# Performance work log

Measured on AMD Instinct MI355X. Metric: run time of the kernel, lower is better.

Reference implementation:

```python
import jax, jax.numpy as jnp
import numpy as np

N, E, E_LG, H, KGE, NUM_GRAPHS, N_ITER = 100000, 500000, 1000000, 128, 128, 1024, 2
EPS = 1e-5

def _prelu(x, a):
    return jnp.where(x >= 0, x, a * x)

def _seg_mean(vals, idx, num):
    s = jax.ops.segment_sum(vals, idx, num_segments=num)
    c = jax.ops.segment_sum(jnp.ones((vals.shape[0],), vals.dtype), idx, num_segments=num)
    return s / jnp.maximum(c, 1.0)[:, None]

def setup_inputs() -> dict:
    key = jax.random.key(0)
    ks = jax.random.split(key, 16)
    sc = 1.0 / np.sqrt(H)
    inp = {
        "x": jax.random.normal(ks[0], (N, H), jnp.float32),
        "edge_attr": jax.random.normal(ks[1], (E, H), jnp.float32),
        "edge_index": jax.random.randint(ks[2], (2, E), 0, N),
        "batch": jnp.sort(jax.random.randint(ks[3], (N,), 0, NUM_GRAPHS)),
        "line_graph_edge_index": jax.random.randint(ks[4], (2, E_LG), 0, E),
        # edge_update_net: Linear + PReLU + BatchNorm1d (eval mode)
        "W1": jax.random.normal(ks[5], (H, H), jnp.float32) * sc,
        "b1": jnp.zeros((H,), jnp.float32),
        "a1": jnp.full((1,), 0.25, jnp.float32),
        "bn_gamma": jnp.ones((H,), jnp.float32),
        "bn_beta": jnp.zeros((H,), jnp.float32),
        "bn_mean": jnp.zeros((H,), jnp.float32),
        "bn_var": jnp.ones((H,), jnp.float32),
        # GRU (single layer, single step)
        "w_ih": jax.random.normal(ks[6], (3 * H, H), jnp.float32) * sc,
        "w_hh": jax.random.normal(ks[7], (3 * H, H), jnp.float32) * sc,
        "b_ih": jnp.zeros((3 * H,), jnp.float32),
        "b_hh": jnp.zeros((3 * H,), jnp.float32),
        # DynamicAttention net
        "Wa1": jax.random.normal(ks[8], (H // 2, H), jnp.float32) * sc,
        "ba1": jnp.zeros((H // 2,), jnp.float32),
        "a2": jnp.full((1,), 0.25, jnp.float32),
        "Wa2": jax.random.normal(ks[9], (1, H // 2), jnp.float32) * (1.0 / np.sqrt(H // 2)),
        "ba2": jnp.zeros((1,), jnp.float32),
        # readout
        "Wr": jax.random.normal(ks[10], (KGE, H), jnp.float32) * sc,
        "br": jnp.zeros((KGE,), jnp.float32),
    }
    return inp

def reference(x, edge_attr, W1, b1, a1, bn_gamma, bn_beta, bn_mean, bn_var,
              w_ih, w_hh, b_ih, b_hh, Wa1, ba1, a2, Wa2, ba2, Wr, br,
              edge_index, batch, line_graph_edge_index):
    src, dst = edge_index[0], edge_index[1]
    l_src, l_dst = line_graph_edge_index[0], line_graph_edge_index[1]
    h = x  # GRU hidden state [N, H]
    for _ in range(N_ITER):
        # edge-to-edge message passing (node_to_edge_proj is Identity here)
        fused = edge_attr + (x[src] + x[dst]) * 0.5  # [E, H]
        agg = _seg_mean(fused[l_src], l_dst, E)      # scatter-mean over line graph
        upd = _prelu(agg @ W1.T + b1, a1)
        upd = (upd - bn_mean) * jax.lax.rsqrt(bn_var + EPS) * bn_gamma + bn_beta
        fused = fused + upd
        node_updates = _seg_mean(fused, dst, N)      # [N, H]
        # single GRU step
        gi = node_updates @ w_ih.T + b_ih
        gh = h @ w_hh.T + b_hh
        gi_r, gi_z, gi_n = jnp.split(gi, 3, axis=-1)
        gh_r, gh_z, gh_n = jnp.split(gh, 3, axis=-1)
        r = jax.nn.sigmoid(gi_r + gh_r)
        z = jax.nn.sigmoid(gi_z + gh_z)
        n = jnp.tanh(gi_n + r * gh_n)
        h = (1.0 - z) * n + z * h
        x = h
    # dynamic attention: per-graph scalar gate
    graph_repr = _seg_mean(x, batch, NUM_GRAPHS)     # [G, H]
    attn = jax.nn.sigmoid(_prelu(graph_repr @ Wa1.T + ba1, a2) @ Wa2.T + ba2)  # [G, 1]
    attended = x * attn[batch]
    graph_emb = jax.ops.segment_sum(attended, batch, num_segments=NUM_GRAPHS)
    graph_emb = graph_emb @ Wr.T + br
    return (x, graph_emb)
```

## Files before the change

### kernel.cpp

```cpp
#include <hip/hip_runtime.h>
#include <stdint.h>

#define H 128
#define G_NUM 1024
#define BN_EPS 1e-5f

typedef unsigned int uint;
typedef unsigned short ushort;
typedef __attribute__((ext_vector_type(8))) __bf16 bf16x8;
typedef __attribute__((ext_vector_type(8))) ushort ushort8;
typedef __attribute__((ext_vector_type(4))) float f32x4;

__device__ __forceinline__ float b2f(ushort u){ return __uint_as_float(((uint)u) << 16); }
__device__ __forceinline__ ushort f2b(float f){
    uint u = __float_as_uint(f);
    u += 0x7FFFu + ((u >> 16) & 1u);
    return (ushort)(u >> 16);
}
__device__ __forceinline__ float ldf(const void* p, size_t i, int bf){
    return bf ? b2f(((const ushort*)p)[i]) : ((const float*)p)[i];
}
__device__ __forceinline__ int swz(int r, int byte_in_row){
    return (r * 256 + byte_in_row) ^ ((r & 7) << 4);
}

__global__ void k_probe(const uint* __restrict__ gamma_bits, int* __restrict__ flag){
    if (threadIdx.x == 0 && blockIdx.x == 0)
        *flag = (gamma_bits[0] == 0x3F803F80u) ? 1 : 0;
}

__global__ __launch_bounds__(256) void k_count2(const int* __restrict__ lgi, const int* __restrict__ ei,
                                                int* __restrict__ cnt, int ELG, int E){
    int t = blockIdx.x * 256 + threadIdx.x;
    if (t < ELG) atomicAdd(&cnt[lgi[ELG + t]], 1);
    else { int t2 = t - ELG; if (t2 < E) atomicAdd(&cnt[E + ei[E + t2]], 1); }
}
__global__ __launch_bounds__(256) void k_scan_reduce(const int* __restrict__ cnt, int* __restrict__ bsum, int n){
    int base = blockIdx.x * 1024;
    int s = 0;
    for (int i = threadIdx.x; i < 1024; i += 256){ int idx = base + i; s += (idx < n) ? cnt[idx] : 0; }
    __shared__ int r[256];
    r[threadIdx.x] = s; __syncthreads();
    for (int o = 128; o > 0; o >>= 1){ if (threadIdx.x < o) r[threadIdx.x] += r[threadIdx.x + o]; __syncthreads(); }
    if (threadIdx.x == 0) bsum[blockIdx.x] = r[0];
}
__global__ __launch_bounds__(256) void k_scan_mid(int* __restrict__ bsum, int nb){
    __shared__ int ts[256];
    int tid = threadIdx.x;
    int loc[4]; int s = 0;
    #pragma unroll
    for (int j = 0; j < 4; j++){
        int idx = tid * 4 + j;
        loc[j] = s;
        s += (idx < nb) ? bsum[idx] : 0;
    }
    ts[tid] = s; __syncthreads();
    for (int o = 1; o < 256; o <<= 1){
        int v = (tid >= o) ? ts[tid - o] : 0;
        __syncthreads();
        ts[tid] += v;
        __syncthreads();
    }
    int texcl = ts[tid] - s;
    #pragma unroll
    for (int j = 0; j < 4; j++){
        int idx = tid * 4 + j;
        if (idx < nb) bsum[idx] = texcl + loc[j];
    }
}
__global__ __launch_bounds__(256) void k_scan_final(const int* __restrict__ cnt, const int* __restrict__ bsum,
                                                    int* __restrict__ off, int n){
    __shared__ int ts[256];
    int base = blockIdx.x * 1024;
    int tid = threadIdx.x;
    int loc[4]; int s = 0;
    #pragma unroll
    for (int j = 0; j < 4; j++){
        int idx = base + tid * 4 + j;
        loc[j] = s;
        s += (idx < n) ? cnt[idx] : 0;
    }
    ts[tid] = s; __syncthreads();
    for (int o = 1; o < 256; o <<= 1){
        int v = (tid >= o) ? ts[tid - o] : 0;
        __syncthreads();
        ts[tid] += v;
        __syncthreads();
    }
    int texcl = ts[tid] - s + bsum[blockIdx.x];
    #pragma unroll
    for (int j = 0; j < 4; j++){
        int idx = base + tid * 4 + j;
        if (idx < n) off[idx] = texcl + loc[j];
    }
}
__global__ void k_sent1(int* __restrict__ off, int idx, int val){
    if (threadIdx.x == 0) off[idx] = val;
}
__global__ __launch_bounds__(256) void k_fill2(const int* __restrict__ lgi, const int* __restrict__ ei,
                                               const int* __restrict__ off, int* __restrict__ cur,
                                               int* __restrict__ list, int ELG, int E){
    int t = blockIdx.x * 256 + threadIdx.x;
    if (t < ELG){
        int k = lgi[ELG + t];
        int pos = atomicAdd(&cur[k], 1);
        list[off[k] + pos] = lgi[t];
    } else {
        int t2 = t - ELG;
        if (t2 < E){
            int k = E + ei[E + t2];
            int pos = atomicAdd(&cur[k], 1);
            list[off[k] + pos] = t2;
        }
    }
}
__global__ void k_zero2(ushort* __restrict__ a, ushort* __restrict__ b, size_t off){
    int t = threadIdx.x;
    a[off + t] = 0; b[off + t] = 0;
}
__global__ __launch_bounds__(256) void k_cvt_bf(const void* __restrict__ in, ushort* __restrict__ out,
                                                int n, const int* __restrict__ flag){
    int t = blockIdx.x * 256 + threadIdx.x;
    if (t >= n) return;
    if (*flag) out[t] = ((const ushort*)in)[t];
    else       out[t] = f2b(((const float*)in)[t]);
}
__global__ __launch_bounds__(256) void k_wcvt(const void* __restrict__ W1, const void* __restrict__ wih,
                                              const void* __restrict__ whh,
                                              ushort* __restrict__ W1bf, ushort* __restrict__ wihbf,
                                              ushort* __restrict__ whhbf, const int* __restrict__ flag){
    int t = blockIdx.x * 256 + threadIdx.x;
    int bf = *flag;
    if (t < 16384) W1bf[t] = bf ? ((const ushort*)W1)[t] : f2b(((const float*)W1)[t]);
    else if (t < 65536){ int i = t - 16384; wihbf[i] = bf ? ((const ushort*)wih)[i] : f2b(((const float*)wih)[i]); }
    else if (t < 114688){ int i = t - 65536; whhbf[i] = bf ? ((const ushort*)whh)[i] : f2b(((const float*)whh)[i]); }
}
__global__ __launch_bounds__(256) void k_transpose(const void* __restrict__ in, float* __restrict__ out,
                                                   int R, int C, const int* __restrict__ flag){
    int t = blockIdx.x * 256 + threadIdx.x;
    if (t >= R * C) return;
    int bf = *flag;
    int r = t / C, c = t - r * C;
    out[c * R + r] = ldf(in, t, bf);
}
__global__ void k_params(const void* b1, const void* a1, const void* gam, const void* bet,
                         const void* mean, const void* var, const void* bih, const void* bhh,
                         float* __restrict__ ep, float* __restrict__ bi, float* __restrict__ bh,
                         const int* __restrict__ flag){
    int t = threadIdx.x; int bf = *flag;
    bi[t] = ldf(bih, t, bf);
    bh[t] = ldf(bhh, t, bf);
    if (t < 128){
        ep[t]       = ldf(b1, t, bf);
        ep[128 + t] = rsqrtf(ldf(var, t, bf) + BN_EPS) * ldf(gam, t, bf);
        ep[256 + t] = ldf(mean, t, bf);
        ep[384 + t] = ldf(bet, t, bf);
    }
    if (t == 0) ep[512] = ldf(a1, 0, bf);
}
__global__ __launch_bounds__(256) void k_store_h(const ushort* __restrict__ hb, void* __restrict__ out,
                                                 int n, const int* __restrict__ flag){
    int t = blockIdx.x * 256 + threadIdx.x;
    if (t >= n) return;
    ushort v = hb[t];
    if (*flag) ((ushort*)out)[t] = v;
    else       ((float*) out)[t] = b2f(v);
}

__global__ __launch_bounds__(256) void k_fused(const void* __restrict__ ea, const ushort* __restrict__ hb,
                                               const int* __restrict__ ei, ushort* __restrict__ fused,
                                               int E, const int* __restrict__ flag){
    int t = blockIdx.x * 256 + threadIdx.x;
    if (t >= E * 16) return;
    int bf = *flag;
    int e = t >> 4, ch = (t & 15) * 8;
    int s = ei[e], d = ei[E + e];
    ushort8 hs = *(const ushort8*)(hb + (size_t)s * H + ch);
    ushort8 hd = *(const ushort8*)(hb + (size_t)d * H + ch);
    size_t base = (size_t)e * H + ch;
    float av[8];
    if (bf){
        ushort8 a = *(const ushort8*)((const ushort*)ea + base);
        #pragma unroll
        for (int j = 0; j < 8; j++) av[j] = b2f(a[j]);
    } else {
        float4 a0 = *(const float4*)((const float*)ea + base);
        float4 a1 = *(const float4*)((const float*)ea + base + 4);
        av[0] = a0.x; av[1] = a0.y; av[2] = a0.z; av[3] = a0.w;
        av[4] = a1.x; av[5] = a1.y; av[6] = a1.z; av[7] = a1.w;
    }
    ushort8 o;
    #pragma unroll
    for (int j = 0; j < 8; j++) o[j] = f2b(av[j] + 0.5f * (b2f(hs[j]) + b2f(hd[j])));
    *(ushort8*)(fused + base) = o;
}

__global__ __launch_bounds__(256) void k_agg_gemm(const ushort* __restrict__ fused,
                                                  const int* __restrict__ off_cat, const int* __restrict__ list,
                                                  const ushort* __restrict__ W1bf, const float* __restrict__ ep,
                                                  ushort* __restrict__ fused2, int E, int LMAX){
    __shared__ __attribute__((aligned(16))) char As[32 * 256];
    __shared__ int offL[33];
    int tid = threadIdx.x, wid = tid >> 6, lane = tid & 63;
    int r0 = blockIdx.x * 32;
    if (tid < 33) offL[tid] = off_cat[r0 + tid];
    __syncthreads();
    int l16 = lane >> 4, ch16 = lane & 15;
    int rA = wid * 8 + l16, rB = rA + 4;
    int baseA = offL[rA], degA = offL[rA + 1] - baseA;
    int baseB = offL[rB], degB = offL[rB + 1] - baseB;
    int dm = max(degA, degB);
    float accA[8] = {}, accB[8] = {};
    #pragma unroll 4
    for (int i = 0; i < dm; i++){
        int liA = baseA + i; liA = (liA < LMAX) ? liA : (LMAX - 1);
        int liB = baseB + i; liB = (liB < LMAX) ? liB : (LMAX - 1);
        int sA = list[liA];
        int sB = list[liB];
        sA = (i < degA) ? sA : E;
        sB = (i < degB) ? sB : E;
        ushort8 vA = *(const ushort8*)(fused + (size_t)sA * H + ch16 * 8);
        ushort8 vB = *(const ushort8*)(fused + (size_t)sB * H + ch16 * 8);
        #pragma unroll
        for (int j = 0; j < 8; j++){ accA[j] += b2f(vA[j]); accB[j] += b2f(vB[j]); }
    }
    float invA = 1.f / fmaxf((float)degA, 1.f);
    float invB = 1.f / fmaxf((float)degB, 1.f);
    ushort8 oA, oB;
    #pragma unroll
    for (int j = 0; j < 8; j++){ oA[j] = f2b(accA[j] * invA); oB[j] = f2b(accB[j] * invB); }
    *(ushort8*)(As + swz(rA, ch16 * 16)) = oA;
    *(ushort8*)(As + swz(rB, ch16 * 16)) = oB;
    __syncthreads();
    int lrow = lane & 15, lhi = lane >> 4;
    f32x4 acc[2][2] = {};
    #pragma unroll
    for (int ks = 0; ks < 4; ks++){
        bf16x8 afr[2];
        #pragma unroll
        for (int rt = 0; rt < 2; rt++)
            afr[rt] = *(const bf16x8*)(As + swz(rt * 16 + lrow, ks * 64 + lhi * 16));
        #pragma unroll
        for (int cc = 0; cc < 2; cc++){
            int c = (2 * wid + cc) * 16 + lrow;
            bf16x8 bfr = *(const bf16x8*)(W1bf + (size_t)c * H + ks * 32 + lhi * 8);
            #pragma unroll
            for (int rt = 0; rt < 2; rt++)
                acc[cc][rt] = __builtin_amdgcn_mfma_f32_16x16x32_bf16(afr[rt], bfr, acc[cc][rt], 0, 0, 0);
        }
    }
    __syncthreads();
    float aa = ep[512];
    #pragma unroll
    for (int cc = 0; cc < 2; cc++){
        int c = (2 * wid + cc) * 16 + lrow;
        float bb = ep[c], sc = ep[128 + c], mb = ep[256 + c], be = ep[384 + c];
        #pragma unroll
        for (int rt = 0; rt < 2; rt++)
            #pragma unroll
            for (int rg = 0; rg < 4; rg++){
                int r = rt * 16 + lhi * 4 + rg;
                float u = acc[cc][rt][rg] + bb;
                u = (u >= 0.f) ? u : aa * u;
                u = (u - mb) * sc + be;
                *(ushort*)(As + swz(r, c * 2)) = f2b(u);
            }
    }
    __syncthreads();
    #pragma unroll
    for (int q = 0; q < 2; q++){
        int r = (q == 0) ? rA : rB;
        size_t gbase = (size_t)(r0 + r) * H + ch16 * 8;
        ushort8 f = *(const ushort8*)(fused + gbase);
        ushort8 u = *(const ushort8*)(As + swz(r, ch16 * 16));
        ushort8 o;
        #pragma unroll
        for (int j = 0; j < 8; j++) o[j] = f2b(b2f(f[j]) + b2f(u[j]));
        *(ushort8*)(fused2 + gbase) = o;
    }
}

__global__ __launch_bounds__(256) void k_gru(const ushort* __restrict__ fused2,
                                             const int* __restrict__ off_cat, const int* __restrict__ list,
                                             ushort* __restrict__ hb,
                                             const ushort* __restrict__ wihbf, const ushort* __restrict__ whhbf,
                                             const float* __restrict__ bi, const float* __restrict__ bh,
                                             int N, int EZ, int LMAX){
    __shared__ __attribute__((aligned(16))) char NUs[32 * 256];
    __shared__ __attribute__((aligned(16))) char HHs[32 * 256];
    __shared__ int offL[33];
    int tid = threadIdx.x, wid = tid >> 6, lane = tid & 63;
    int r0 = blockIdx.x * 32;
    if (tid < 33) offL[tid] = off_cat[r0 + tid];
    int l16 = lane >> 4, ch16 = lane & 15;
    int rA = wid * 8 + l16, rB = rA + 4;
    *(ushort8*)(HHs + swz(rA, ch16 * 16)) = *(const ushort8*)(hb + (size_t)(r0 + rA) * H + ch16 * 8);
    *(ushort8*)(HHs + swz(rB, ch16 * 16)) = *(const ushort8*)(hb + (size_t)(r0 + rB) * H + ch16 * 8);
    __syncthreads();
    int baseA = offL[rA], degA = offL[rA + 1] - baseA;
    int baseB = offL[rB], degB = offL[rB + 1] - baseB;
    int dm = max(degA, degB);
    float accA[8] = {}, accB[8] = {};
    #pragma unroll 4
    for (int i = 0; i < dm; i++){
        int liA = baseA + i; liA = (liA < LMAX) ? liA : (LMAX - 1);
        int liB = baseB + i; liB = (liB < LMAX) ? liB : (LMAX - 1);
        int sA = list[liA];
        int sB = list[liB];
        sA = (i < degA) ? sA : EZ;
        sB = (i < degB) ? sB : EZ;
        ushort8 vA = *(const ushort8*)(fused2 + (size_t)sA * H + ch16 * 8);
        ushort8 vB = *(const ushort8*)(fused2 + (size_t)sB * H + ch16 * 8);
        #pragma unroll
        for (int j = 0; j < 8; j++){ accA[j] += b2f(vA[j]); accB[j] += b2f(vB[j]); }
    }
    float invA = 1.f / fmaxf((float)degA, 1.f);
    float invB = 1.f / fmaxf((float)degB, 1.f);
    ushort8 oA, oB;
    #pragma unroll
    for (int j = 0; j < 8; j++){ oA[j] = f2b(accA[j] * invA); oB[j] = f2b(accB[j] * invB); }
    *(ushort8*)(NUs + swz(rA, ch16 * 16)) = oA;
    *(ushort8*)(NUs + swz(rB, ch16 * 16)) = oB;
    __syncthreads();
    int lrow = lane & 15, lhi = lane >> 4;
    ushort hnew[2][2][4];
    #pragma unroll
    for (int b = 0; b < 2; b++){
        f32x4 aI[3][2] = {}, aH[3][2] = {};
        #pragma unroll
        for (int ks = 0; ks < 4; ks++){
            bf16x8 fN[2], fH[2];
            #pragma unroll
            for (int rt = 0; rt < 2; rt++){
                int addr = swz(rt * 16 + lrow, ks * 64 + lhi * 16);
                fN[rt] = *(const bf16x8*)(NUs + addr);
                fH[rt] = *(const bf16x8*)(HHs + addr);
            }
            #pragma unroll
            for (int g = 0; g < 3; g++){
                int c = g * 128 + (wid + 4 * b) * 16 + lrow;
                bf16x8 bI = *(const bf16x8*)(wihbf + (size_t)c * H + ks * 32 + lhi * 8);
                bf16x8 bH = *(const bf16x8*)(whhbf + (size_t)c * H + ks * 32 + lhi * 8);
                #pragma unroll
                for (int rt = 0; rt < 2; rt++){
                    aI[g][rt] = __builtin_amdgcn_mfma_f32_16x16x32_bf16(fN[rt], bI, aI[g][rt], 0, 0, 0);
                    aH[g][rt] = __builtin_amdgcn_mfma_f32_16x16x32_bf16(fH[rt], bH, aH[g][rt], 0, 0, 0);
                }
            }
        }
        int c = (wid + 4 * b) * 16 + lrow;
        float bir = bi[c], biz = bi[128 + c], bin = bi[256 + c];
        float bhr = bh[c], bhz = bh[128 + c], bhn = bh[256 + c];
        #pragma unroll
        for (int rt = 0; rt < 2; rt++)
            #pragma unroll
            for (int rg = 0; rg < 4; rg++){
                int r = rt * 16 + lhi * 4 + rg;
                float gr = aI[0][rt][rg] + bir + aH[0][rt][rg] + bhr;
                float gz = aI[1][rt][rg] + biz + aH[1][rt][rg] + bhz;
                float rv = 1.f / (1.f + __expf(-gr));
                float zv = 1.f / (1.f + __expf(-gz));
                float nv = tanhf(aI[2][rt][rg] + bin + rv * (aH[2][rt][rg] + bhn));
                float hold = b2f(*(const ushort*)(HHs + swz(r, c * 2)));
                hnew[b][rt][rg] = f2b((1.f - zv) * nv + zv * hold);
            }
    }
    __syncthreads();
    #pragma unroll
    for (int b = 0; b < 2; b++){
        int c = (wid + 4 * b) * 16 + lrow;
        #pragma unroll
        for (int rt = 0; rt < 2; rt++)
            #pragma unroll
            for (int rg = 0; rg < 4; rg++){
                int r = rt * 16 + lhi * 4 + rg;
                *(ushort*)(NUs + swz(r, c * 2)) = hnew[b][rt][rg];
            }
    }
    __syncthreads();
    *(ushort8*)(hb + (size_t)(r0 + rA) * H + ch16 * 8) = *(const ushort8*)(NUs + swz(rA, ch16 * 16));
    *(ushort8*)(hb + (size_t)(r0 + rB) * H + ch16 * 8) = *(const ushort8*)(NUs + swz(rB, ch16 * 16));
}

__global__ __launch_bounds__(256) void k_gbounds(const int* __restrict__ batch, int* __restrict__ gs, int N, int G){
    int g = blockIdx.x * 256 + threadIdx.x;
    if (g > G) return;
    int lo = 0, hi = N;
    while (lo < hi){ int mid = (lo + hi) >> 1; if (batch[mid] < g) lo = mid + 1; else hi = mid; }
    gs[g] = lo;
}
__global__ __launch_bounds__(256) void k_graph_sum(const ushort* __restrict__ hb, const int* __restrict__ gs,
                                                   float* __restrict__ gsum){
    int g = blockIdx.x, c = threadIdx.x & 127, half = threadIdx.x >> 7;
    int s = gs[g], e = gs[g + 1];
    float acc0 = 0.f, acc1 = 0.f;
    int r = s + half;
    for (; r + 2 < e; r += 4){
        acc0 += b2f(hb[(size_t)r * H + c]);
        acc1 += b2f(hb[(size_t)(r + 2) * H + c]);
    }
    for (; r < e; r += 2) acc0 += b2f(hb[(size_t)r * H + c]);
    __shared__ float tmp[128];
    if (half == 1) tmp[c] = acc0 + acc1;
    __syncthreads();
    if (half == 0) gsum[(size_t)g * H + c] = acc0 + acc1 + tmp[c];
}
__global__ void k_attn(const float* __restrict__ gsum, const int* __restrict__ gs,
                       const void* __restrict__ Wa1, const void* __restrict__ ba1,
                       const void* __restrict__ a2, const void* __restrict__ Wa2,
                       const void* __restrict__ ba2, float* __restrict__ attn, const int* __restrict__ flag){
    int g = blockIdx.x;
    int j = threadIdx.x;
    int bf = *flag;
    float inv = 1.0f / fmaxf((float)(gs[g + 1] - gs[g]), 1.0f);
    __shared__ float R[H];
    for (int i = j; i < H; i += 64) R[i] = gsum[(size_t)g * H + i] * inv;
    __syncthreads();
    float t = 0.f;
    for (int k = 0; k < H; k++) t += R[k] * ldf(Wa1, (size_t)j * H + k, bf);
    t += ldf(ba1, j, bf);
    float al = ldf(a2, 0, bf);
    t = (t >= 0.f) ? t : al * t;
    float p = t * ldf(Wa2, j, bf);
    #pragma unroll
    for (int o = 32; o > 0; o >>= 1) p += __shfl_down(p, o);
    if (j == 0) attn[g] = 1.f / (1.f + __expf(-(p + ldf(ba2, 0, bf))));
}
__global__ __launch_bounds__(256) void k_graph_gemm(const float* __restrict__ gsum, const float* __restrict__ attn,
                                                    const float* __restrict__ WrT,
                                                    const void* __restrict__ br, void* __restrict__ out,
                                                    size_t obase, const int* __restrict__ flag){
    __shared__ float A[8 * H];
    int bf = *flag;
    int r0 = blockIdx.x * 8;
    for (int i = threadIdx.x; i < 8 * H; i += 256){
        int r = i >> 7;
        A[i] = gsum[(size_t)(r0 + r) * H + (i & 127)] * attn[r0 + r];
    }
    __syncthreads();
    int c = threadIdx.x & 127;
    int rr = (threadIdx.x >> 7) * 4;
    float acc[4] = {0, 0, 0, 0};
    for (int k = 0; k < H; k++){
        float w = WrT[k * H + c];
        #pragma unroll
        for (int j = 0; j < 4; j++) acc[j] += A[(rr + j) * H + k] * w;
    }
    float bb = ldf(br, c, bf);
    for (int j = 0; j < 4; j++){
        size_t idx = obase + (size_t)(r0 + rr + j) * H + c;
        float v = acc[j] + bb;
        if (bf) ((ushort*)out)[idx] = f2b(v);
        else    ((float*) out)[idx] = v;
    }
}

extern "C" void kernel_launch(void* const* d_in, const int* in_sizes, int n_in,
                              void* d_out, int out_size, void* d_ws, size_t ws_size,
                              hipStream_t stream)
{
    const void* x    = d_in[0];
    const void* ea   = d_in[1];
    const int*  ei   = (const int*)d_in[2];
    const int*  batch= (const int*)d_in[3];
    const int*  lgi  = (const int*)d_in[4];
    const void* W1   = d_in[5];
    const void* b1   = d_in[6];
    const void* a1   = d_in[7];
    const void* bng  = d_in[8];
    const void* bnb  = d_in[9];
    const void* bnm  = d_in[10];
    const void* bnv  = d_in[11];
    const void* wih  = d_in[12];
    const void* whh  = d_in[13];
    const void* bih  = d_in[14];
    const void* bhh  = d_in[15];
    const void* Wa1  = d_in[16];
    const void* ba1  = d_in[17];
    const void* a2   = d_in[18];
    const void* Wa2  = d_in[19];
    const void* ba2  = d_in[20];
    const void* Wr   = d_in[21];
    const void* br   = d_in[22];

    const int N   = in_sizes[0] / H;
    const int E   = in_sizes[1] / H;
    const int ELG = in_sizes[4] / 2;
    const int G   = G_NUM;
    const int NK  = E + N;
    const int nb  = (NK + 1023) / 1024;

    char* ws = (char*)d_ws;
    size_t off = 0;
    auto alloc = [&](size_t b) -> void* { void* p = ws + off; off += (b + 255) & ~(size_t)255; return p; };
    int*    flag    = (int*)   alloc(256);
    ushort* hb      = (ushort*)alloc((size_t)N * H * 2);
    ushort* fused   = (ushort*)alloc((size_t)(E + 1) * H * 2);
    ushort* fused2  = (ushort*)alloc((size_t)(E + 1) * H * 2);
    int*    zreg    = (int*)   alloc((size_t)(2 * NK) * 4);
    int*    cnt_cat = zreg;
    int*    cur_cat = zreg + NK;
    int*    off_cat = (int*)   alloc((size_t)(NK + 1) * 4);
    int*    list_cat= (int*)   alloc((size_t)(ELG + E) * 4);
    int*    bsum    = (int*)   alloc((size_t)(nb + 8) * 4);
    int*    gs      = (int*)   alloc((size_t)(G + 1) * 4);
    ushort* W1bf    = (ushort*)alloc(128 * 128 * 2);
    ushort* wihbf   = (ushort*)alloc(384 * 128 * 2);
    ushort* whhbf   = (ushort*)alloc(384 * 128 * 2);
    float*  ep      = (float*) alloc(513 * 4);
    float*  bi      = (float*) alloc(384 * 4);
    float*  bh      = (float*) alloc(384 * 4);
    float*  WrT     = (float*) alloc(128 * 128 * 4);
    float*  gsum    = (float*) alloc((size_t)G * H * 4);
    float*  attn    = (float*) alloc((size_t)G * 4);

    k_probe<<<1, 64, 0, stream>>>((const uint*)bng, flag);

    hipMemsetAsync(zreg, 0, (size_t)(2 * NK) * 4, stream);
    k_count2<<<(ELG + E + 255) / 256, 256, 0, stream>>>(lgi, ei, cnt_cat, ELG, E);
    k_scan_reduce<<<nb, 256, 0, stream>>>(cnt_cat, bsum, NK);
    k_scan_mid<<<1, 256, 0, stream>>>(bsum, nb);
    k_scan_final<<<nb, 256, 0, stream>>>(cnt_cat, bsum, off_cat, NK);
    k_sent1<<<1, 64, 0, stream>>>(off_cat, NK, ELG + E);
    k_fill2<<<(ELG + E + 255) / 256, 256, 0, stream>>>(lgi, ei, off_cat, cur_cat, list_cat, ELG, E);
    k_zero2<<<1, 128, 0, stream>>>(fused, fused2, (size_t)E * H);

    k_wcvt<<<(114688 + 255) / 256, 256, 0, stream>>>(W1, wih, whh, W1bf, wihbf, whhbf, flag);
    k_params<<<1, 384, 0, stream>>>(b1, a1, bng, bnb, bnm, bnv, bih, bhh, ep, bi, bh, flag);
    k_transpose<<<(128 * 128 + 255) / 256, 256, 0, stream>>>(Wr, WrT, 128, 128, flag);

    k_cvt_bf<<<(N * H + 255) / 256, 256, 0, stream>>>(x, hb, N * H, flag);

    for (int it = 0; it < 2; it++){
        k_fused<<<(E * 16 + 255) / 256, 256, 0, stream>>>(ea, hb, ei, fused, E, flag);
        k_agg_gemm<<<(E + 31) / 32, 256, 0, stream>>>(fused, off_cat, list_cat, W1bf, ep, fused2, E, ELG);
        k_gru<<<(N + 31) / 32, 256, 0, stream>>>(fused2, off_cat + E, list_cat, hb, wihbf, whhbf, bi, bh, N, E, ELG + E);
    }

    k_gbounds<<<(G + 256) / 256, 256, 0, stream>>>(batch, gs, N, G);
    k_graph_sum<<<G, 256, 0, stream>>>(hb, gs, gsum);
    k_attn<<<G, 64, 0, stream>>>(gsum, gs, Wa1, ba1, a2, Wa2, ba2, attn, flag);
    k_graph_gemm<<<G / 8, 256, 0, stream>>>(gsum, attn, WrT, br, d_out, (size_t)N * H, flag);
    k_store_h<<<(N * H + 255) / 256, 256, 0, stream>>>(hb, d_out, N * H, flag);
}
```

Before: 1.012 ms.

## Merge small setup kernels and vectorize bf16 gather accumulation with wave-uniform trip count

Folds the dtype probe, parameter prep, sentinel write and padding-row zeroing into one setup kernel, and moves the Wr transpose into the weight-conversion kernel. This cuts several tiny launches from the stream. The gather loops in the aggregation and GRU kernels now unpack bf16 pairs into packed float2 accumulators. Their loop bound is the maximum degree across the wave, so the trip count is uniform and the unroll factor drops from 4 to 2. The wave-wide maximum adds padded iterations for rows with fewer neighbours.

```diff
diff --git a/kernel.cpp b/kernel.cpp
--- a/kernel.cpp
+++ b/kernel.cpp
@@ -10,6 +10,7 @@
 typedef __attribute__((ext_vector_type(8))) __bf16 bf16x8;
 typedef __attribute__((ext_vector_type(8))) ushort ushort8;
 typedef __attribute__((ext_vector_type(4))) float f32x4;
+typedef __attribute__((ext_vector_type(2))) float f32x2;
 
 __device__ __forceinline__ float b2f(ushort u){ return __uint_as_float(((uint)u) << 16); }
 __device__ __forceinline__ ushort f2b(float f){
@@ -24,9 +25,31 @@
     return (r * 256 + byte_in_row) ^ ((r & 7) << 4);
 }
 
-__global__ void k_probe(const uint* __restrict__ gamma_bits, int* __restrict__ flag){
-    if (threadIdx.x == 0 && blockIdx.x == 0)
-        *flag = (gamma_bits[0] == 0x3F803F80u) ? 1 : 0;
+__global__ void k_setup_small(const uint* __restrict__ gamma_bits,
+                              const void* b1, const void* a1, const void* gam, const void* bet,
+                              const void* mean, const void* var, const void* bih, const void* bhh,
+                              float* __restrict__ ep, float* __restrict__ bi, float* __restrict__ bh,
+                              int* __restrict__ flag, ushort* __restrict__ fz1, ushort* __restrict__ fz2,
+                              size_t zoff, int* __restrict__ off_cat, int nk_idx, int sent_val){
+    __shared__ int bfs;
+    int t = threadIdx.x;
+    if (t == 0){
+        int f = (gamma_bits[0] == 0x3F803F80u) ? 1 : 0;
+        *flag = f; bfs = f;
+        off_cat[nk_idx] = sent_val;
+    }
+    __syncthreads();
+    int bf = bfs;
+    bi[t] = ldf(bih, t, bf);
+    bh[t] = ldf(bhh, t, bf);
+    if (t < 128){
+        ep[t]       = ldf(b1, t, bf);
+        ep[128 + t] = rsqrtf(ldf(var, t, bf) + BN_EPS) * ldf(gam, t, bf);
+        ep[256 + t] = ldf(mean, t, bf);
+        ep[384 + t] = ldf(bet, t, bf);
+        fz1[zoff + t] = 0; fz2[zoff + t] = 0;
+    }
+    if (t == 0) ep[512] = ldf(a1, 0, bf);
 }
 
 __global__ __launch_bounds__(256) void k_count2(const int* __restrict__ lgi, const int* __restrict__ ei,
@@ -93,9 +116,6 @@
         int idx = base + tid * 4 + j;
         if (idx < n) off[idx] = texcl + loc[j];
     }
-}
-__global__ void k_sent1(int* __restrict__ off, int idx, int val){
-    if (threadIdx.x == 0) off[idx] = val;
 }
 __global__ __launch_bounds__(256) void k_fill2(const int* __restrict__ lgi, const int* __restrict__ ei,
                                                const int* __restrict__ off, int* __restrict__ cur,
@@ -114,10 +134,6 @@
         }
     }
 }
-__global__ void k_zero2(ushort* __restrict__ a, ushort* __restrict__ b, size_t off){
-    int t = threadIdx.x;
-    a[off + t] = 0; b[off + t] = 0;
-}
 __global__ __launch_bounds__(256) void k_cvt_bf(const void* __restrict__ in, ushort* __restrict__ out,
                                                 int n, const int* __restrict__ flag){
     int t = blockIdx.x * 256 + threadIdx.x;
@@ -126,37 +142,16 @@
     else       out[t] = f2b(((const float*)in)[t]);
 }
 __global__ __launch_bounds__(256) void k_wcvt(const void* __restrict__ W1, const void* __restrict__ wih,
-                                              const void* __restrict__ whh,
+                                              const void* __restrict__ whh, const void* __restrict__ Wr,
                                               ushort* __restrict__ W1bf, ushort* __restrict__ wihbf,
-                                              ushort* __restrict__ whhbf, const int* __restrict__ flag){
+                                              ushort* __restrict__ whhbf, float* __restrict__ WrT,
+                                              const int* __restrict__ flag){
     int t = blockIdx.x * 256 + threadIdx.x;
     int bf = *flag;
     if (t < 16384) W1bf[t] = bf ? ((const ushort*)W1)[t] : f2b(((const float*)W1)[t]);
     else if (t < 65536){ int i = t - 16384; wihbf[i] = bf ? ((const ushort*)wih)[i] : f2b(((const float*)wih)[i]); }
     else if (t < 114688){ int i = t - 65536; whhbf[i] = bf ? ((const ushort*)whh)[i] : f2b(((const float*)whh)[i]); }
-}
-__global__ __launch_bounds__(256) void k_transpose(const void* __restrict__ in, float* __restrict__ out,
-                                                   int R, int C, const int* __restrict__ flag){
-    int t = blockIdx.x * 256 + threadIdx.x;
-    if (t >= R * C) return;
-    int bf = *flag;
-    int r = t / C, c = t - r * C;
-    out[c * R + r] = ldf(in, t, bf);
-}
-__global__ void k_params(const void* b1, const void* a1, const void* gam, const void* bet,
-                         const void* mean, const void* var, const void* bih, const void* bhh,
-                         float* __restrict__ ep, float* __restrict__ bi, float* __restrict__ bh,
-                         const int* __restrict__ flag){
-    int t = threadIdx.x; int bf = *flag;
-    bi[t] = ldf(bih, t, bf);
-    bh[t] = ldf(bhh, t, bf);
-    if (t < 128){
-        ep[t]       = ldf(b1, t, bf);
-        ep[128 + t] = rsqrtf(ldf(var, t, bf) + BN_EPS) * ldf(gam, t, bf);
-        ep[256 + t] = ldf(mean, t, bf);
-        ep[384 + t] = ldf(bet, t, bf);
-    }
-    if (t == 0) ep[512] = ldf(a1, 0, bf);
+    else if (t < 131072){ int i = t - 114688; int r = i >> 7, c = i & 127; WrT[c * 128 + r] = ldf(Wr, i, bf); }
 }
 __global__ __launch_bounds__(256) void k_store_h(const ushort* __restrict__ hb, void* __restrict__ out,
                                                  int n, const int* __restrict__ flag){
@@ -210,8 +205,10 @@
     int baseA = offL[rA], degA = offL[rA + 1] - baseA;
     int baseB = offL[rB], degB = offL[rB + 1] - baseB;
     int dm = max(degA, degB);
-    float accA[8] = {}, accB[8] = {};
-    #pragma unroll 4
+    #pragma unroll
+    for (int o = 32; o > 0; o >>= 1) dm = max(dm, __shfl_xor(dm, o));
+    f32x2 accA[4] = {}, accB[4] = {};
+    #pragma unroll 2
     for (int i = 0; i < dm; i++){
         int liA = baseA + i; liA = (liA < LMAX) ? liA : (LMAX - 1);
         int liB = baseB + i; liB = (liB < LMAX) ? liB : (LMAX - 1);
@@ -219,16 +216,26 @@
         int sB = list[liB];
         sA = (i < degA) ? sA : E;
         sB = (i < degB) ? sB : E;
-        ushort8 vA = *(const ushort8*)(fused + (size_t)sA * H + ch16 * 8);
-        ushort8 vB = *(const ushort8*)(fused + (size_t)sB * H + ch16 * 8);
-        #pragma unroll
-        for (int j = 0; j < 8; j++){ accA[j] += b2f(vA[j]); accB[j] += b2f(vB[j]); }
+        uint4 wA = *(const uint4*)(fused + (size_t)sA * H + ch16 * 8);
+        uint4 wB = *(const uint4*)(fused + (size_t)sB * H + ch16 * 8);
+        uint wa[4] = {wA.x, wA.y, wA.z, wA.w};
+        uint wb[4] = {wB.x, wB.y, wB.z, wB.w};
+        #pragma unroll
+        for (int k2 = 0; k2 < 4; k2++){
+            f32x2 va, vb;
+            va.x = __uint_as_float(wa[k2] << 16); va.y = __uint_as_float(wa[k2] & 0xFFFF0000u);
+            vb.x = __uint_as_float(wb[k2] << 16); vb.y = __uint_as_float(wb[k2] & 0xFFFF0000u);
+            accA[k2] += va; accB[k2] += vb;
+        }
     }
     float invA = 1.f / fmaxf((float)degA, 1.f);
     float invB = 1.f / fmaxf((float)degB, 1.f);
     ushort8 oA, oB;
     #pragma unroll
-    for (int j = 0; j < 8; j++){ oA[j] = f2b(accA[j] * invA); oB[j] = f2b(accB[j] * invB); }
+    for (int k2 = 0; k2 < 4; k2++){
+        oA[2 * k2] = f2b(accA[k2].x * invA); oA[2 * k2 + 1] = f2b(accA[k2].y * invA);
+        oB[2 * k2] = f2b(accB[k2].x * invB); oB[2 * k2 + 1] = f2b(accB[k2].y * invB);
+    }
     *(ushort8*)(As + swz(rA, ch16 * 16)) = oA;
     *(ushort8*)(As + swz(rB, ch16 * 16)) = oB;
     __syncthreads();
@@ -300,8 +307,10 @@
     int baseA = offL[rA], degA = offL[rA + 1] - baseA;
     int baseB = offL[rB], degB = offL[rB + 1] - baseB;
     int dm = max(degA, degB);
-    float accA[8] = {}, accB[8] = {};
-    #pragma unroll 4
+    #pragma unroll
+    for (int o = 32; o > 0; o >>= 1) dm = max(dm, __shfl_xor(dm, o));
+    f32x2 accA[4] = {}, accB[4] = {};
+    #pragma unroll 2
     for (int i = 0; i < dm; i++){
         int liA = baseA + i; liA = (liA < LMAX) ? liA : (LMAX - 1);
         int liB = baseB + i; liB = (liB < LMAX) ? liB : (LMAX - 1);
@@ -309,16 +318,26 @@
         int sB = list[liB];
         sA = (i < degA) ? sA : EZ;
         sB = (i < degB) ? sB : EZ;
-        ushort8 vA = *(const ushort8*)(fused2 + (size_t)sA * H + ch16 * 8);
-        ushort8 vB = *(const ushort8*)(fused2 + (size_t)sB * H + ch16 * 8);
-        #pragma unroll
-        for (int j = 0; j < 8; j++){ accA[j] += b2f(vA[j]); accB[j] += b2f(vB[j]); }
+        uint4 wA = *(const uint4*)(fused2 + (size_t)sA * H + ch16 * 8);
+        uint4 wB = *(const uint4*)(fused2 + (size_t)sB * H + ch16 * 8);
+        uint wa[4] = {wA.x, wA.y, wA.z, wA.w};
+        uint wb[4] = {wB.x, wB.y, wB.z, wB.w};
+        #pragma unroll
+        for (int k2 = 0; k2 < 4; k2++){
+            f32x2 va, vb;
+            va.x = __uint_as_float(wa[k2] << 16); va.y = __uint_as_float(wa[k2] & 0xFFFF0000u);
+            vb.x = __uint_as_float(wb[k2] << 16); vb.y = __uint_as_float(wb[k2] & 0xFFFF0000u);
+            accA[k2] += va; accB[k2] += vb;
+        }
     }
     float invA = 1.f / fmaxf((float)degA, 1.f);
     float invB = 1.f / fmaxf((float)degB, 1.f);
     ushort8 oA, oB;
     #pragma unroll
-    for (int j = 0; j < 8; j++){ oA[j] = f2b(accA[j] * invA); oB[j] = f2b(accB[j] * invB); }
+    for (int k2 = 0; k2 < 4; k2++){
+        oA[2 * k2] = f2b(accA[k2].x * invA); oA[2 * k2 + 1] = f2b(accA[k2].y * invA);
+        oB[2 * k2] = f2b(accB[k2].x * invB); oB[2 * k2 + 1] = f2b(accB[k2].y * invB);
+    }
     *(ushort8*)(NUs + swz(rA, ch16 * 16)) = oA;
     *(ushort8*)(NUs + swz(rB, ch16 * 16)) = oB;
     __syncthreads();
@@ -514,20 +533,18 @@
     float*  gsum    = (float*) alloc((size_t)G * H * 4);
     float*  attn    = (float*) alloc((size_t)G * 4);
 
-    k_probe<<<1, 64, 0, stream>>>((const uint*)bng, flag);
+    k_setup_small<<<1, 384, 0, stream>>>((const uint*)bng, b1, a1, bng, bnb, bnm, bnv, bih, bhh,
+                                         ep, bi, bh, flag, fused, fused2, (size_t)E * H,
+                                         off_cat, NK, ELG + E);
 
     hipMemsetAsync(zreg, 0, (size_t)(2 * NK) * 4, stream);
     k_count2<<<(ELG + E + 255) / 256, 256, 0, stream>>>(lgi, ei, cnt_cat, ELG, E);
     k_scan_reduce<<<nb, 256, 0, stream>>>(cnt_cat, bsum, NK);
     k_scan_mid<<<1, 256, 0, stream>>>(bsum, nb);
     k_scan_final<<<nb, 256, 0, stream>>>(cnt_cat, bsum, off_cat, NK);
-    k_sent1<<<1, 64, 0, stream>>>(off_cat, NK, ELG + E);
     k_fill2<<<(ELG + E + 255) / 256, 256, 0, stream>>>(lgi, ei, off_cat, cur_cat, list_cat, ELG, E);
-    k_zero2<<<1, 128, 0, stream>>>(fused, fused2, (size_t)E * H);
-
-    k_wcvt<<<(114688 + 255) / 256, 256, 0, stream>>>(W1, wih, whh, W1bf, wihbf, whhbf, flag);
-    k_params<<<1, 384, 0, stream>>>(b1, a1, bng, bnb, bnm, bnv, bih, bhh, ep, bi, bh, flag);
-    k_transpose<<<(128 * 128 + 255) / 256, 256, 0, stream>>>(Wr, WrT, 128, 128, flag);
+
+    k_wcvt<<<(131072 + 255) / 256, 256, 0, stream>>>(W1, wih, whh, Wr, W1bf, wihbf, whhbf, WrT, flag);
 
     k_cvt_bf<<<(N * H + 255) / 256, 256, 0, stream>>>(x, hb, N * H, flag);
 
```

After: 965.4 us. 4.6% less time.
